# Performance work log

Measured on AMD Instinct MI355X. Metric: run time of the kernel, lower is better.

## Reference

```python
import jax, jax.numpy as jnp
import numpy as np

B, P, G, E = 2, 16, 128, 96
C110, C011, C001 = 4, 2, 1
N, CO = 128, 2

def _pw(x, W, b):
    """1x1 conv of any spatial rank == pointwise channel mixing."""
    y = jnp.einsum('oc,bc...->bo...', W, x)
    return y + b.reshape((1, -1) + (1,) * (y.ndim - 2))

def _hidden(s110, s011, s001, Ws, bs):
    # s110:[B,C,P,G,1]  s011:[B,C,1,G,E]  s001:[B,C,1,1,E]
    # sub-stream order: [110 full, 110 pool-P, 110 pool-G, 011 full, 011 pool-G, 011 pool-E, 001]
    t110 = s110[..., 0]         # [B,C,P,G]
    t011 = s011[:, :, 0]        # [B,C,G,E]
    t001 = s001[:, :, 0, 0]     # [B,C,E]
    s = (_pw(t110, Ws[0], bs[0])[..., None]
         + _pw(t110.max(axis=2), Ws[1], bs[1])[:, :, None, :, None]
         + _pw(t110.max(axis=3), Ws[2], bs[2])[:, :, :, None, None]
         + _pw(t011, Ws[3], bs[3])[:, :, None, :, :]
         + _pw(t011.max(axis=2), Ws[4], bs[4])[:, :, None, None, :]
         + _pw(t011.max(axis=3), Ws[5], bs[5])[:, :, None, :, None]
         + _pw(t001, Ws[6], bs[6])[:, :, None, None, :])
    s = jax.nn.leaky_relu(s)    # [B,N,P,G,E]
    return (jnp.max(s, axis=4, keepdims=True),
            jnp.max(s, axis=2, keepdims=True),
            jnp.max(s, axis=(2, 3), keepdims=True))

def _forward(x110, x011, x001, W0_110, b0_110, W0_011, b0_011, W0_001, b0_001, W1, b1, Wact, bact, Wcrit, bcrit):
    Ws0 = [W0_110[0], W0_110[1], W0_110[2], W0_011[0], W0_011[1], W0_011[2], W0_001]
    bs0 = [b0_110[0], b0_110[1], b0_110[2], b0_011[0], b0_011[1], b0_011[2], b0_001]
    s110, s011, s001 = _hidden(x110, x011, x001, Ws0, bs0)
    s110, s011, s001 = _hidden(s110, s011, s001, list(W1), list(b1))
    t110 = s110[..., 0]  # [B,N,P,G]
    # actor head: eliminate G,E via mean pooling (dim_elimination_max_pooling=False)
    a110 = _pw(t110.mean(axis=3), Wact[0], bact[0])              # [B,CO,P]
    a011 = _pw(s011.mean(axis=(3, 4)), Wact[1], bact[1])         # [B,CO,1]
    a001 = _pw(s001[:, :, :, 0].mean(axis=3), Wact[2], bact[2])  # [B,CO,1]
    actions = jax.nn.leaky_relu(a110 + a011 + a001)              # [B,CO,P]
    # critic head: eliminate G via mean pooling
    c110 = _pw(t110.mean(axis=3), Wcrit[0], bcrit[0])            # [B,CO,P]
    c011 = _pw(s011[:, :, 0].mean(axis=2), Wcrit[1], bcrit[1])   # [B,CO,E]
    c001 = _pw(s001[:, :, 0, 0], Wcrit[2], bcrit[2])             # [B,CO,E]
    v = jax.nn.leaky_relu(c110[:, :, :, None] + (c011 + c001)[:, :, None, :])  # [B,CO,P,E]
    v110 = v.max(axis=3).sum(axis=2)  # stream (1,1,0): max over E, sum over P
    v011 = v.max(axis=2).sum(axis=2)  # streams (0,1,1) and (0,0,1) coincide numerically
    values = (2.0 + v110 + 2.0 * v011).reshape(-1)  # python sum(l, 2) starts at 2
    return actions, values

def setup_inputs() -> dict:
    key = jax.random.key(0)
    ks = jax.random.split(key, 12)
    f32 = jnp.float32
    def w(k, shape, fan):
        return jax.random.normal(k, shape, f32) / np.float32(np.sqrt(fan))
    return {
        'x110': jax.random.normal(ks[0], (B, C110, P, G, 1), f32),
        'x011': jax.random.normal(ks[1], (B, C011, 1, G, E), f32),
        'x001': jax.random.normal(ks[2], (B, C001, 1, 1, E), f32),
        'W0_110': w(ks[3], (3, N, C110), C110), 'b0_110': jnp.zeros((3, N), f32),
        'W0_011': w(ks[4], (3, N, C011), C011), 'b0_011': jnp.zeros((3, N), f32),
        'W0_001': w(ks[5], (N, C001), C001),    'b0_001': jnp.zeros((N,), f32),
        'W1':     w(ks[6], (7, N, N), N),       'b1':     jnp.zeros((7, N), f32),
        'Wact':   w(ks[7], (3, CO, N), N),      'bact':   jnp.zeros((3, CO), f32),
        'Wcrit':  w(ks[8], (3, CO, N), N),      'bcrit':  jnp.zeros((3, CO), f32),
    }

def reference(x110, x011, x001, W0_110, b0_110, W0_011, b0_011, W0_001, b0_001, W1, b1, Wact, bact, Wcrit, bcrit):
    return _forward(x110, x011, x001, W0_110, b0_110, W0_011, b0_011, W0_001, b0_001, W1, b1, Wact, bact, Wcrit, bcrit)
```

## Files before the change

kernel.cpp:

```cpp
#include <hip/hip_runtime.h>
#include <math.h>

#define DEVI __device__ __forceinline__

constexpr int B = 2, P = 16, G = 128, E = 96, N = 128, CO = 2;

DEVI float lrelu(float x) { return x > 0.f ? x : 0.01f * x; }

constexpr int OFF_U1     = 0;
constexpr int OFF_V1     = OFF_U1 + 524288;
constexpr int OFF_MAXPU0 = OFF_V1 + 3145728;
constexpr int OFF_MAXEV0 = OFF_MAXPU0 + 32768;
constexpr int OFF_MP110  = OFF_MAXEV0 + 32768;
constexpr int OFF_MG110  = OFF_MP110 + 32768;
constexpr int OFF_S001A  = OFF_MG110 + 4096;
constexpr int OFF_RMP    = OFF_S001A + 24576;
constexpr int OFF_RMG    = OFF_RMP + 1024;
constexpr int OFF_RME    = OFF_RMG + 128;
constexpr int OFF_RMG011 = OFF_RME + 512;
constexpr int OFF_M110   = OFF_RMG011 + 384;
constexpr int OFF_M011E  = OFF_M110 + 4096;
constexpr int OFF_S001B  = OFF_M011E + 24576;
constexpr int OFF_WT     = OFF_S001B + 24576;

__global__ void __launch_bounds__(256) k_layer0(
    const float* __restrict__ x110, const float* __restrict__ x011,
    const float* __restrict__ x001,
    const float* __restrict__ W0_110, const float* __restrict__ b0_110,
    const float* __restrict__ W0_011, const float* __restrict__ b0_011,
    const float* __restrict__ W0_001, const float* __restrict__ b0_001,
    const float* __restrict__ W1,
    float* __restrict__ maxpU0g, float* __restrict__ maxeV0g,
    float* __restrict__ mp110, float* __restrict__ mg110,
    float* __restrict__ s001a,
    float* __restrict__ rmpG, float* __restrict__ rmgG,
    float* __restrict__ rmeG, float* __restrict__ rmg011G,
    float* __restrict__ wT) {
  __shared__ float xs[4 * 16 * 128];
  __shared__ float v0[128 * 97];
  __shared__ float u0[16 * 128];
  __shared__ float rmp[512], rmgS[64], rme[256], rmg011L[192];
  __shared__ float mpu[128], mev[128], part[256];
  const int bn = blockIdx.x, b = bn >> 7, n = bn & 127, tid = threadIdx.x;

  {
    const float4* xsrc = (const float4*)(x110 + (size_t)b * 8192);
    float4* xdst = (float4*)xs;
#pragma unroll
    for (int k = 0; k < 8; k++) xdst[tid + k * 256] = xsrc[tid + k * 256];
  }
  __syncthreads();
  for (int i = tid; i < 512; i += 256) {
    int c = i >> 7, g = i & 127;
    float m = -INFINITY;
    for (int p = 0; p < P; p++) m = fmaxf(m, xs[(c * 16 + p) * 128 + g]);
    rmp[i] = m;
  }
  if (tid < 64) {
    int c = tid >> 4, p = tid & 15;
    float m = -INFINITY;
    for (int g = 0; g < G; g++) m = fmaxf(m, xs[(c * 16 + p) * 128 + g]);
    rmgS[tid] = m;
  }
  {
    int c = tid >> 7, g = tid & 127;
    const float4* r = (const float4*)(x011 + ((size_t)(b * 2 + c) * 128 + g) * 96);
    float m = -INFINITY;
#pragma unroll
    for (int j = 0; j < 24; j++) {
      float4 v = r[j];
      m = fmaxf(m, fmaxf(fmaxf(v.x, v.y), fmaxf(v.z, v.w)));
    }
    rme[tid] = m;
  }
  if (tid < 192) {
    int c = tid / 96, e = tid % 96;
    const float* pp = x011 + ((size_t)(b * 2 + c) * 128) * 96 + e;
    float m = -INFINITY;
    for (int g = 0; g < G; g++) m = fmaxf(m, pp[g * 96]);
    rmg011L[tid] = m;
  }
  __syncthreads();
  float w0[4], w1[4], w2[4];
#pragma unroll
  for (int cc = 0; cc < 4; cc++) {
    w0[cc] = W0_110[n * 4 + cc];
    w1[cc] = W0_110[512 + n * 4 + cc];
    w2[cc] = W0_110[1024 + n * 4 + cc];
  }
  float we0 = W0_011[512 + n * 2], we1 = W0_011[512 + n * 2 + 1];
  float bu = b0_110[n] + b0_110[128 + n] + b0_110[256 + n] + b0_011[256 + n];
  float vw00 = W0_011[n * 2], vw01 = W0_011[n * 2 + 1];
  float vw10 = W0_011[256 + n * 2], vw11 = W0_011[256 + n * 2 + 1];
  float w001 = W0_001[n];
  float bv = b0_011[n] + b0_011[128 + n] + b0_001[n];

#pragma unroll
  for (int k = 0; k < 8; k++) {
    int i = tid + k * 256, p = i >> 7, g = i & 127;
    float acc = bu + we0 * rme[g] + we1 * rme[128 + g];
#pragma unroll
    for (int cc = 0; cc < 4; cc++)
      acc += w0[cc] * xs[(cc * 16 + p) * 128 + g] + w1[cc] * rmp[cc * 128 + g]
           + w2[cc] * rmgS[cc * 16 + p];
    u0[i] = acc;
  }
  {
    const float* xa = x011 + (size_t)(b * 2) * 12288;
    const float* xb = xa + 12288;
    const float* xc = x001 + b * 96;
    for (int k = 0; k < 48; k++) {
      int i = tid + k * 256;
      int g = i / 96, e = i - g * 96;
      float val = bv + vw00 * xa[i] + vw01 * xb[i]
                + vw10 * rmg011L[e] + vw11 * rmg011L[96 + e] + w001 * xc[e];
      v0[g * 97 + e] = val;
    }
  }
  __syncthreads();
  if (tid < 128) {
    float m = -INFINITY;
    for (int p = 0; p < P; p++) m = fmaxf(m, u0[p * 128 + tid]);
    mpu[tid] = m;
    maxpU0g[bn * 128 + tid] = m;
  }
  {
    int g = tid & 127, h = tid >> 7;
    const float* r = &v0[g * 97 + h * 48];
    float m = -INFINITY;
    for (int j = 0; j < 48; j++) m = fmaxf(m, r[j]);
    part[tid] = m;
  }
  __syncthreads();
  if (tid < 128) {
    float m = fmaxf(part[tid], part[128 + tid]);
    mev[tid] = m;
    maxeV0g[bn * 128 + tid] = m;
    mp110[bn * 128 + tid] = lrelu(mpu[tid] + m);
  }
  __syncthreads();
  {
    int p = tid >> 4, ch = tid & 15;
    float m = -INFINITY;
    for (int g = ch * 8; g < ch * 8 + 8; g++)
      m = fmaxf(m, u0[p * 128 + g] + mev[g]);
    part[tid] = m;
  }
  if (tid < 96) {
    float m = -INFINITY;
    for (int g = 0; g < G; g++) m = fmaxf(m, mpu[g] + v0[g * 97 + tid]);
    s001a[bn * 96 + tid] = lrelu(m);
  }
  __syncthreads();
  if (tid < 16) {
    float m = -INFINITY;
    for (int ch = 0; ch < 16; ch++) m = fmaxf(m, part[tid * 16 + ch]);
    mg110[bn * 16 + tid] = lrelu(m);
  }
  if (n == 0) {
    for (int i = tid; i < 512; i += 256) rmpG[b * 512 + i] = rmp[i];
    if (tid < 64) rmgG[b * 64 + tid] = rmgS[tid];
    rmeG[b * 256 + tid] = rme[tid];
    if (tid < 192) rmg011G[b * 192 + tid] = rmg011L[tid];
  }
  {
    const int gt = bn * 256 + tid;
#pragma unroll
    for (int it = 0; it < 2; it++) {
      int idx = gt + it * 65536;
      if (idx < 81920) {
        int m = idx >> 14, r = idx & 16383;
        int c = r >> 7, nn = r & 127;
        float v;
        if (m == 0)      v = W1[nn * 128 + c];
        else if (m == 1) v = W1[16384 + nn * 128 + c] + W1[5 * 16384 + nn * 128 + c];
        else if (m == 2) v = W1[2 * 16384 + nn * 128 + c];
        else if (m == 3) v = W1[3 * 16384 + nn * 128 + c];
        else             v = W1[4 * 16384 + nn * 128 + c] + W1[6 * 16384 + nn * 128 + c];
        wT[idx] = v;
      }
    }
  }
}

__global__ void __launch_bounds__(512) k_layer1c(
    const float* __restrict__ x110, const float* __restrict__ x011,
    const float* __restrict__ x001,
    const float* __restrict__ W0_110, const float* __restrict__ b0_110,
    const float* __restrict__ W0_011, const float* __restrict__ b0_011,
    const float* __restrict__ W0_001, const float* __restrict__ b0_001,
    const float* __restrict__ maxpU0g, const float* __restrict__ maxeV0g,
    const float* __restrict__ rmpG, const float* __restrict__ rmgG,
    const float* __restrict__ rmeG, const float* __restrict__ rmg011G,
    const float* __restrict__ wT,
    float* __restrict__ U1, float* __restrict__ V1) {
  __shared__ float s110c[128 * 16];
  __shared__ float s011c[128 * 96];
  __shared__ float W0L110[1536], W0L011[768], W0L001[128];
  __shared__ float busum[128], bvsum[128], mpu[128], mev[128];
  __shared__ float x011row[192], rmg011s[192], x001s[96];
  __shared__ float x110col[64], rmg110p[64], rmp4[4], rme2[2];
  const int blk = blockIdx.x;
  const int b = blk >> 7, g = blk & 127;
  const int tid = threadIdx.x;

  for (int i = tid; i < 1536; i += 512) W0L110[i] = W0_110[i];
  for (int i = tid; i < 768; i += 512) W0L011[i] = W0_011[i];
  if (tid < 128) {
    W0L001[tid] = W0_001[tid];
    busum[tid] = b0_110[tid] + b0_110[128 + tid] + b0_110[256 + tid]
               + b0_011[256 + tid];
    bvsum[tid] = b0_011[tid] + b0_011[128 + tid] + b0_001[tid];
    mpu[tid] = maxpU0g[(b * 128 + tid) * 128 + g];
    mev[tid] = maxeV0g[(b * 128 + tid) * 128 + g];
  } else if (tid >= 256 && tid < 448) {
    int i = tid - 256;
    int c = i / 96, e = i % 96;
    x011row[i] = x011[((size_t)(b * 2 + c) * 128 + g) * 96 + e];
    rmg011s[i] = rmg011G[b * 192 + i];
  } else if (tid >= 448 && tid < 512) {
    int i = tid - 448;
    int c = i >> 4, p = i & 15;
    x110col[i] = x110[((size_t)(b * 4 + c) * 16 + p) * 128 + g];
    rmg110p[i] = rmgG[b * 64 + i];
  } else if (tid >= 128 && tid < 224) {
    x001s[tid - 128] = x001[b * 96 + tid - 128];
  } else if (tid >= 224 && tid < 228) {
    rmp4[tid - 224] = rmpG[(b * 4 + tid - 224) * 128 + g];
  } else if (tid >= 228 && tid < 230) {
    rme2[tid - 228] = rmeG[(b * 2 + tid - 228) * 128 + g];
  }
  __syncthreads();

#pragma unroll
  for (int k = 0; k < 4; k++) {
    int i = tid + k * 512, c = i >> 4, p = i & 15;
    float acc = busum[c] + W0L011[512 + c * 2] * rme2[0]
              + W0L011[512 + c * 2 + 1] * rme2[1];
#pragma unroll
    for (int cc = 0; cc < 4; cc++)
      acc += W0L110[c * 4 + cc] * x110col[cc * 16 + p]
           + W0L110[512 + c * 4 + cc] * rmp4[cc]
           + W0L110[1024 + c * 4 + cc] * rmg110p[cc * 16 + p];
    s110c[i] = lrelu(acc + mev[c]);
  }
  for (int k = 0; k < 24; k++) {
    int i = tid + k * 512;
    int c = i / 96, e = i - c * 96;
    float v = bvsum[c]
            + W0L011[c * 2] * x011row[e] + W0L011[c * 2 + 1] * x011row[96 + e]
            + W0L011[256 + c * 2] * rmg011s[e]
            + W0L011[256 + c * 2 + 1] * rmg011s[96 + e]
            + W0L001[c] * x001s[e];
    s011c[i] = lrelu(v + mpu[c]);
  }
  __syncthreads();

  const float* w0T = wT;
  const float* w3T = wT + 3 * 16384;

  {
    int n = tid & 127, ph = tid >> 7;
    float a[4] = {0.f, 0.f, 0.f, 0.f};
    for (int c = 0; c < 128; c++) {
      float w0v = w0T[c * 128 + n];
      float4 s = *(const float4*)&s110c[c * 16 + ph * 4];
      a[0] += w0v * s.x; a[1] += w0v * s.y; a[2] += w0v * s.z; a[3] += w0v * s.w;
    }
    float* dst = U1 + ((size_t)((b * 128 + g) * 16 + ph * 4)) * 128 + n;
#pragma unroll
    for (int j = 0; j < 4; j++) dst[j * 128] = a[j];
  }
  {
    int n0 = (tid >> 3) * 2, e0 = (tid & 7) * 12;
    float4 aA[3], aB[3];
#pragma unroll
    for (int k = 0; k < 3; k++) {
      aA[k] = make_float4(0.f, 0.f, 0.f, 0.f);
      aB[k] = make_float4(0.f, 0.f, 0.f, 0.f);
    }
    for (int c = 0; c < 128; c++) {
      float2 wv = *(const float2*)&w3T[c * 128 + n0];
      float4 s0 = *(const float4*)&s011c[c * 96 + e0];
      float4 s1 = *(const float4*)&s011c[c * 96 + e0 + 4];
      float4 s2 = *(const float4*)&s011c[c * 96 + e0 + 8];
      aA[0].x += wv.x * s0.x; aA[0].y += wv.x * s0.y;
      aA[0].z += wv.x * s0.z; aA[0].w += wv.x * s0.w;
      aA[1].x += wv.x * s1.x; aA[1].y += wv.x * s1.y;
      aA[1].z += wv.x * s1.z; aA[1].w += wv.x * s1.w;
      aA[2].x += wv.x * s2.x; aA[2].y += wv.x * s2.y;
      aA[2].z += wv.x * s2.z; aA[2].w += wv.x * s2.w;
      aB[0].x += wv.y * s0.x; aB[0].y += wv.y * s0.y;
      aB[0].z += wv.y * s0.z; aB[0].w += wv.y * s0.w;
      aB[1].x += wv.y * s1.x; aB[1].y += wv.y * s1.y;
      aB[1].z += wv.y * s1.z; aB[1].w += wv.y * s1.w;
      aB[2].x += wv.y * s2.x; aB[2].y += wv.y * s2.y;
      aB[2].z += wv.y * s2.z; aB[2].w += wv.y * s2.w;
    }
    float* dA = V1 + ((size_t)((b * 128 + g) * 128 + n0)) * 96 + e0;
    float* dB = dA + 96;
#pragma unroll
    for (int k = 0; k < 3; k++) {
      *(float4*)(dA + k * 4) = aA[k];
      *(float4*)(dB + k * 4) = aB[k];
    }
  }
}

__global__ void __launch_bounds__(256) k_post1b(
    const float* __restrict__ U1, const float* __restrict__ V1,
    const float* __restrict__ s001a, const float* __restrict__ mp110,
    const float* __restrict__ mg110,
    const float* __restrict__ wT, const float* __restrict__ b1,
    float* __restrict__ m110, float* __restrict__ m011e,
    float* __restrict__ s001b) {
  __shared__ float vrow[128 * 97];
  __shared__ float uU[16 * 128];
  __shared__ float part[256];
  __shared__ float smaxeV[128], smaxpU[128];
  __shared__ float bf[128], eg[96], cp[16];
  const int bn = blockIdx.x, b = bn >> 7, n = bn & 127;
  const int tid = threadIdx.x;
  const float* w15T = wT + 16384;
  const float* w2T  = wT + 2 * 16384;
  const float* w46T = wT + 4 * 16384;

  if (tid < 128) {
    float acc = 0.f;
    for (int c = 0; c < 128; c++)
      acc += w15T[c * 128 + n] * mp110[(b * 128 + c) * 128 + tid];
    bf[tid] = acc;
  } else if (tid < 224) {
    int e = tid - 128;
    float acc = 0.f;
    for (int c = 0; c < 128; c++)
      acc += w46T[c * 128 + n] * s001a[b * 12288 + c * 96 + e];
    eg[e] = acc;
  } else if (tid < 240) {
    int p = tid - 224;
    float acc = 0.f;
    for (int c = 0; c < 128; c++)
      acc += w2T[c * 128 + n] * mg110[(b * 128 + c) * 16 + p];
    cp[p] = acc;
  }
  __syncthreads();
  const float bb = b1[n] + b1[128 + n] + b1[256 + n] + b1[640 + n];
  const float bv = b1[384 + n] + b1[512 + n] + b1[768 + n];

  for (int i = tid; i < 2048; i += 256) {
    int p = i >> 7, g = i & 127;
    uU[i] = U1[((size_t)((b * 128 + g) * 16 + p)) * 128 + n] + bb + cp[p] + bf[g];
  }
#pragma unroll
  for (int k = 0; k < 12; k++) {
    int i4 = tid + k * 256;
    int g = i4 / 24, e4 = i4 - g * 24;
    float4 v = *(const float4*)(V1 + ((size_t)((b * 128 + g) * 128 + n)) * 96 + e4 * 4);
    float* d = &vrow[g * 97 + e4 * 4];
    d[0] = v.x + bv + eg[e4 * 4];
    d[1] = v.y + bv + eg[e4 * 4 + 1];
    d[2] = v.z + bv + eg[e4 * 4 + 2];
    d[3] = v.w + bv + eg[e4 * 4 + 3];
  }
  __syncthreads();
  {
    int g = tid & 127, h = tid >> 7;
    const float* r = &vrow[g * 97 + h * 48];
    float m = -INFINITY;
    for (int j = 0; j < 48; j++) m = fmaxf(m, r[j]);
    part[tid] = m;
  }
  __syncthreads();
  if (tid < 128) {
    smaxeV[tid] = fmaxf(part[tid], part[tid + 128]);
    float mp = -INFINITY;
    for (int p = 0; p < P; p++) mp = fmaxf(mp, uU[p * 128 + tid]);
    smaxpU[tid] = mp;
  }
  __syncthreads();
  if (tid >= 128 && tid < 144) {
    int p = tid - 128;
    float s = 0.f;
    for (int g = 0; g < G; g++)
      s += lrelu(uU[p * 128 + g] + smaxeV[g]);
    m110[bn * 16 + p] = s * (1.f / G);
  }
  if (tid < 96) {
    float s = 0.f, mm = -INFINITY;
    for (int g = 0; g < G; g++) {
      float pre = smaxpU[g] + vrow[g * 97 + tid];
      s += lrelu(pre);
      mm = fmaxf(mm, pre);
    }
    m011e[bn * 96 + tid] = s * (1.f / G);
    s001b[bn * 96 + tid] = lrelu(mm);
  }
}

__global__ void __launch_bounds__(128) k_final(const float* __restrict__ m110,
                                               const float* __restrict__ m011e,
                                               const float* __restrict__ s001,
                                               const float* __restrict__ Wact,
                                               const float* __restrict__ bact,
                                               const float* __restrict__ Wcrit,
                                               const float* __restrict__ bcrit,
                                               float* __restrict__ out) {
  __shared__ float sm011[N], sm001[N], scp[P], sce[E], srow[P], scol[E];
  const int bo = blockIdx.x;
  const int o = bo & 1, b = bo >> 1;
  const int t = threadIdx.x;
  {
    float s1 = 0.f, s2 = 0.f;
    const float* p1 = m011e + (b * N + t) * E;
    const float* p2 = s001 + (b * N + t) * E;
    for (int e = 0; e < E; e++) { s1 += p1[e]; s2 += p2[e]; }
    sm011[t] = s1 * (1.f / E);
    sm001[t] = s2 * (1.f / E);
  }
  __syncthreads();
  if (t < P) {
    const float* wa0 = Wact + o * N;
    const float* wa1 = Wact + (1 * CO + o) * N;
    const float* wa2 = Wact + (2 * CO + o) * N;
    const float* wc0 = Wcrit + o * N;
    float a = 0.f, c = 0.f, aa = 0.f;
    for (int n = 0; n < N; n++) {
      float m = m110[(b * N + n) * P + t];
      a += wa0[n] * m;
      c += wc0[n] * m;
      aa += wa1[n] * sm011[n] + wa2[n] * sm001[n];
    }
    float act = a + aa + bact[o] + bact[CO + o] + bact[2 * CO + o];
    out[(b * CO + o) * P + t] = lrelu(act);
    scp[t] = c + bcrit[o];
  } else if (t < P + E) {
    int e = t - P;
    const float* wc1 = Wcrit + (1 * CO + o) * N;
    const float* wc2 = Wcrit + (2 * CO + o) * N;
    float c = 0.f;
    for (int n = 0; n < N; n++)
      c += wc1[n] * m011e[(b * N + n) * E + e] + wc2[n] * s001[(b * N + n) * E + e];
    sce[e] = c + bcrit[CO + o] + bcrit[2 * CO + o];
  }
  __syncthreads();
  if (t < P) {
    float m = -INFINITY;
    for (int e = 0; e < E; e++) m = fmaxf(m, lrelu(scp[t] + sce[e]));
    srow[t] = m;
  } else if (t < P + E) {
    int e = t - P;
    float m = -INFINITY;
    for (int p = 0; p < P; p++) m = fmaxf(m, lrelu(scp[p] + sce[e]));
    scol[e] = m;
  }
  __syncthreads();
  if (t == 0) {
    float v110 = 0.f, v011 = 0.f;
    for (int p = 0; p < P; p++) v110 += srow[p];
    for (int e = 0; e < E; e++) v011 += scol[e];
    out[B * CO * P + b * CO + o] = 2.f + v110 + 2.f * v011;
  }
}

extern "C" void kernel_launch(void* const* d_in, const int* in_sizes, int n_in,
                              void* d_out, int out_size, void* d_ws, size_t ws_size,
                              hipStream_t stream) {
  const float* x110   = (const float*)d_in[0];
  const float* x011   = (const float*)d_in[1];
  const float* x001   = (const float*)d_in[2];
  const float* W0_110 = (const float*)d_in[3];
  const float* b0_110 = (const float*)d_in[4];
  const float* W0_011 = (const float*)d_in[5];
  const float* b0_011 = (const float*)d_in[6];
  const float* W0_001 = (const float*)d_in[7];
  const float* b0_001 = (const float*)d_in[8];
  const float* W1     = (const float*)d_in[9];
  const float* b1     = (const float*)d_in[10];
  const float* Wact   = (const float*)d_in[11];
  const float* bact   = (const float*)d_in[12];
  const float* Wcrit  = (const float*)d_in[13];
  const float* bcrit  = (const float*)d_in[14];
  float* out = (float*)d_out;
  float* w = (float*)d_ws;

  float* U1     = w + OFF_U1;
  float* V1     = w + OFF_V1;
  float* maxpU0 = w + OFF_MAXPU0;
  float* maxeV0 = w + OFF_MAXEV0;
  float* mp110  = w + OFF_MP110;
  float* mg110  = w + OFF_MG110;
  float* s001a  = w + OFF_S001A;
  float* rmpG   = w + OFF_RMP;
  float* rmgG   = w + OFF_RMG;
  float* rmeG   = w + OFF_RME;
  float* rmg011 = w + OFF_RMG011;
  float* m110   = w + OFF_M110;
  float* m011e  = w + OFF_M011E;
  float* s001b  = w + OFF_S001B;
  float* wT     = w + OFF_WT;

  k_layer0<<<256, 256, 0, stream>>>(x110, x011, x001, W0_110, b0_110, W0_011,
                                    b0_011, W0_001, b0_001, W1,
                                    maxpU0, maxeV0, mp110, mg110, s001a,
                                    rmpG, rmgG, rmeG, rmg011, wT);
  k_layer1c<<<256, 512, 0, stream>>>(x110, x011, x001, W0_110, b0_110, W0_011,
                                     b0_011, W0_001, b0_001,
                                     maxpU0, maxeV0, rmpG, rmgG, rmeG, rmg011,
                                     wT, U1, V1);
  k_post1b<<<256, 256, 0, stream>>>(U1, V1, s001a, mp110, mg110, wT, b1,
                                    m110, m011e, s001b);
  k_final<<<4, 128, 0, stream>>>(m110, m011e, s001b, Wact, bact, Wcrit, bcrit, out);
}
```

Measured before the change: 108.5 us.

## Restructure post-layer kernel to tile 8 channels per block and stage k_final loads in LDS

The per-(b,n) post-processing kernel, which launched 256 blocks each reading a strided 128x96 V1 slice, is replaced by 32 blocks that each handle 8 consecutive channels. They stream G in chunks of 8 through shared memory, so V1 reads become contiguous across n, and they keep running sum and max accumulators in registers. The final kernel now stages m110, m011e and s001 in LDS with coalesced loads instead of doing strided per-thread global reads. The trade is far fewer blocks on a large GPU (32 vs 256), less parallelism and more syncs per block.

```diff
diff --git a/kernel.cpp b/kernel.cpp
--- a/kernel.cpp
+++ b/kernel.cpp
@@ -307,93 +307,128 @@
   }
 }
 
-__global__ void __launch_bounds__(256) k_post1b(
+__global__ void __launch_bounds__(256) k_post2(
     const float* __restrict__ U1, const float* __restrict__ V1,
     const float* __restrict__ s001a, const float* __restrict__ mp110,
     const float* __restrict__ mg110,
     const float* __restrict__ wT, const float* __restrict__ b1,
     float* __restrict__ m110, float* __restrict__ m011e,
     float* __restrict__ s001b) {
-  __shared__ float vrow[128 * 97];
-  __shared__ float uU[16 * 128];
-  __shared__ float part[256];
-  __shared__ float smaxeV[128], smaxpU[128];
-  __shared__ float bf[128], eg[96], cp[16];
-  const int bn = blockIdx.x, b = bn >> 7, n = bn & 127;
+  constexpr int GS = 8;
+  __shared__ float Vt[GS][8][100];
+  __shared__ float Ut[GS][16][9];
+  __shared__ float bfL[8][128];
+  __shared__ float egL[8][96];
+  __shared__ float cpL[8][16];
+  __shared__ float partE[GS][8][4];
+  __shared__ float mxeV[GS][8], mxpU[GS][8];
+  __shared__ float bbL[8], bvL[8];
+  const int blk = blockIdx.x, b = blk >> 4, nc = blk & 15, n0 = nc * 8;
   const int tid = threadIdx.x;
   const float* w15T = wT + 16384;
   const float* w2T  = wT + 2 * 16384;
   const float* w46T = wT + 4 * 16384;
 
-  if (tid < 128) {
+  if (tid < 8) {
+    int n = n0 + tid;
+    bbL[tid] = b1[n] + b1[128 + n] + b1[256 + n] + b1[640 + n];
+    bvL[tid] = b1[384 + n] + b1[512 + n] + b1[768 + n];
+  }
+  {
+    int g = tid & 127, h = tid >> 7;
+    float a0 = 0, a1 = 0, a2 = 0, a3 = 0;
+    for (int c = 0; c < 128; c++) {
+      float m = mp110[(b * 128 + c) * 128 + g];
+      const float* wr = &w15T[c * 128 + n0 + h * 4];
+      a0 += wr[0] * m; a1 += wr[1] * m; a2 += wr[2] * m; a3 += wr[3] * m;
+    }
+    bfL[h * 4 + 0][g] = a0; bfL[h * 4 + 1][g] = a1;
+    bfL[h * 4 + 2][g] = a2; bfL[h * 4 + 3][g] = a3;
+  }
+#pragma unroll
+  for (int k = 0; k < 3; k++) {
+    int s = tid + k * 256;
+    int nn = s / 96, e = s % 96;
     float acc = 0.f;
     for (int c = 0; c < 128; c++)
-      acc += w15T[c * 128 + n] * mp110[(b * 128 + c) * 128 + tid];
-    bf[tid] = acc;
-  } else if (tid < 224) {
-    int e = tid - 128;
+      acc += w46T[c * 128 + n0 + nn] * s001a[b * 12288 + c * 96 + e];
+    egL[nn][e] = acc;
+  }
+  if (tid < 128) {
+    int nn = tid >> 4, p = tid & 15;
     float acc = 0.f;
     for (int c = 0; c < 128; c++)
-      acc += w46T[c * 128 + n] * s001a[b * 12288 + c * 96 + e];
-    eg[e] = acc;
-  } else if (tid < 240) {
-    int p = tid - 224;
-    float acc = 0.f;
-    for (int c = 0; c < 128; c++)
-      acc += w2T[c * 128 + n] * mg110[(b * 128 + c) * 16 + p];
-    cp[p] = acc;
-  }
-  __syncthreads();
-  const float bb = b1[n] + b1[128 + n] + b1[256 + n] + b1[640 + n];
-  const float bv = b1[384 + n] + b1[512 + n] + b1[768 + n];
-
-  for (int i = tid; i < 2048; i += 256) {
-    int p = i >> 7, g = i & 127;
-    uU[i] = U1[((size_t)((b * 128 + g) * 16 + p)) * 128 + n] + bb + cp[p] + bf[g];
-  }
-#pragma unroll
-  for (int k = 0; k < 12; k++) {
-    int i4 = tid + k * 256;
-    int g = i4 / 24, e4 = i4 - g * 24;
-    float4 v = *(const float4*)(V1 + ((size_t)((b * 128 + g) * 128 + n)) * 96 + e4 * 4);
-    float* d = &vrow[g * 97 + e4 * 4];
-    d[0] = v.x + bv + eg[e4 * 4];
-    d[1] = v.y + bv + eg[e4 * 4 + 1];
-    d[2] = v.z + bv + eg[e4 * 4 + 2];
-    d[3] = v.w + bv + eg[e4 * 4 + 3];
-  }
-  __syncthreads();
-  {
-    int g = tid & 127, h = tid >> 7;
-    const float* r = &vrow[g * 97 + h * 48];
-    float m = -INFINITY;
-    for (int j = 0; j < 48; j++) m = fmaxf(m, r[j]);
-    part[tid] = m;
-  }
-  __syncthreads();
+      acc += w2T[c * 128 + n0 + nn] * mg110[(b * 128 + c) * 16 + p];
+    cpL[nn][p] = acc;
+  }
+
+  float accM110 = 0.f;
+  float accSum[3] = {0.f, 0.f, 0.f};
+  float accMax[3] = {-INFINITY, -INFINITY, -INFINITY};
+  const size_t Ubase = (size_t)b * 128 * 16 * 128;
+  const size_t Vbase = (size_t)b * 128 * 128 * 96;
+
+  for (int go = 0; go < 128; go += GS) {
+    __syncthreads();
+#pragma unroll
+    for (int k = 0; k < 24; k++) {
+      int i = tid + k * 256;
+      int gs = i / 768, r = i % 768, nn = r / 96, e = r % 96;
+      float v = V1[Vbase + ((size_t)(go + gs) * 128 + n0 + nn) * 96 + e];
+      Vt[gs][nn][e] = v + bvL[nn] + egL[nn][e];
+    }
+#pragma unroll
+    for (int k = 0; k < 4; k++) {
+      int i = tid + k * 256;
+      int gs = i >> 7, r = i & 127, p = r >> 3, nn = r & 7;
+      float u = U1[Ubase + ((size_t)(go + gs) * 16 + p) * 128 + n0 + nn];
+      Ut[gs][p][nn] = u + bbL[nn] + cpL[nn][p] + bfL[nn][go + gs];
+    }
+    __syncthreads();
+    {
+      int gs = tid >> 5, nn = (tid >> 2) & 7, ec = tid & 3;
+      float m = -INFINITY;
+      for (int e = ec * 24; e < ec * 24 + 24; e++) m = fmaxf(m, Vt[gs][nn][e]);
+      partE[gs][nn][ec] = m;
+    }
+    __syncthreads();
+    if (tid < 64) {
+      int gs = tid >> 3, nn = tid & 7;
+      mxeV[gs][nn] = fmaxf(fmaxf(partE[gs][nn][0], partE[gs][nn][1]),
+                           fmaxf(partE[gs][nn][2], partE[gs][nn][3]));
+      float m = -INFINITY;
+      for (int p = 0; p < 16; p++) m = fmaxf(m, Ut[gs][p][nn]);
+      mxpU[gs][nn] = m;
+    }
+    __syncthreads();
+    if (tid < 128) {
+      int nn = tid >> 4, p = tid & 15;
+#pragma unroll
+      for (int gs = 0; gs < GS; gs++)
+        accM110 += lrelu(Ut[gs][p][nn] + mxeV[gs][nn]);
+    }
+#pragma unroll
+    for (int k = 0; k < 3; k++) {
+      int s = tid + k * 256;
+      int nn = s / 96, e = s % 96;
+#pragma unroll
+      for (int gs = 0; gs < GS; gs++) {
+        float pre = mxpU[gs][nn] + Vt[gs][nn][e];
+        accSum[k] += lrelu(pre);
+        accMax[k] = fmaxf(accMax[k], pre);
+      }
+    }
+  }
   if (tid < 128) {
-    smaxeV[tid] = fmaxf(part[tid], part[tid + 128]);
-    float mp = -INFINITY;
-    for (int p = 0; p < P; p++) mp = fmaxf(mp, uU[p * 128 + tid]);
-    smaxpU[tid] = mp;
-  }
-  __syncthreads();
-  if (tid >= 128 && tid < 144) {
-    int p = tid - 128;
-    float s = 0.f;
-    for (int g = 0; g < G; g++)
-      s += lrelu(uU[p * 128 + g] + smaxeV[g]);
-    m110[bn * 16 + p] = s * (1.f / G);
-  }
-  if (tid < 96) {
-    float s = 0.f, mm = -INFINITY;
-    for (int g = 0; g < G; g++) {
-      float pre = smaxpU[g] + vrow[g * 97 + tid];
-      s += lrelu(pre);
-      mm = fmaxf(mm, pre);
-    }
-    m011e[bn * 96 + tid] = s * (1.f / G);
-    s001b[bn * 96 + tid] = lrelu(mm);
+    int nn = tid >> 4, p = tid & 15;
+    m110[(b * 128 + n0 + nn) * 16 + p] = accM110 * (1.f / G);
+  }
+#pragma unroll
+  for (int k = 0; k < 3; k++) {
+    int s = tid + k * 256;
+    int nn = s / 96, e = s % 96;
+    m011e[(b * 128 + n0 + nn) * 96 + e] = accSum[k] * (1.f / G);
+    s001b[(b * 128 + n0 + nn) * 96 + e] = lrelu(accMax[k]);
   }
 }
 
@@ -405,17 +440,50 @@
                                                const float* __restrict__ Wcrit,
                                                const float* __restrict__ bcrit,
                                                float* __restrict__ out) {
-  __shared__ float sm011[N], sm001[N], scp[P], sce[E], srow[P], scol[E];
+  __shared__ float buf[128][97];
+  __shared__ float m110s[128][17];
+  __shared__ float sm011[N], sm001[N], sce1[E], sce[E], scp[P], srow[P], scol[E];
   const int bo = blockIdx.x;
   const int o = bo & 1, b = bo >> 1;
   const int t = threadIdx.x;
-  {
-    float s1 = 0.f, s2 = 0.f;
-    const float* p1 = m011e + (b * N + t) * E;
-    const float* p2 = s001 + (b * N + t) * E;
-    for (int e = 0; e < E; e++) { s1 += p1[e]; s2 += p2[e]; }
-    sm011[t] = s1 * (1.f / E);
-    sm001[t] = s2 * (1.f / E);
+
+#pragma unroll
+  for (int k = 0; k < 16; k++) {
+    int i = t + k * 128;
+    m110s[i >> 4][i & 15] = m110[b * 2048 + i];
+  }
+  for (int k = 0; k < 96; k++) {
+    int i = t + k * 128;
+    buf[i / 96][i % 96] = m011e[b * 12288 + i];
+  }
+  __syncthreads();
+  {
+    float s = 0.f;
+    for (int e = 0; e < E; e++) s += buf[t][e];
+    sm011[t] = s * (1.f / E);
+  }
+  if (t < 96) {
+    const float* wc1 = Wcrit + (1 * CO + o) * N;
+    float c = 0.f;
+    for (int n = 0; n < N; n++) c += wc1[n] * buf[n][t];
+    sce1[t] = c;
+  }
+  __syncthreads();
+  for (int k = 0; k < 96; k++) {
+    int i = t + k * 128;
+    buf[i / 96][i % 96] = s001[b * 12288 + i];
+  }
+  __syncthreads();
+  {
+    float s = 0.f;
+    for (int e = 0; e < E; e++) s += buf[t][e];
+    sm001[t] = s * (1.f / E);
+  }
+  if (t < 96) {
+    const float* wc2 = Wcrit + (2 * CO + o) * N;
+    float c = 0.f;
+    for (int n = 0; n < N; n++) c += wc2[n] * buf[n][t];
+    sce[t] = sce1[t] + c + bcrit[CO + o] + bcrit[2 * CO + o];
   }
   __syncthreads();
   if (t < P) {
@@ -425,7 +493,7 @@
     const float* wc0 = Wcrit + o * N;
     float a = 0.f, c = 0.f, aa = 0.f;
     for (int n = 0; n < N; n++) {
-      float m = m110[(b * N + n) * P + t];
+      float m = m110s[n][t];
       a += wa0[n] * m;
       c += wc0[n] * m;
       aa += wa1[n] * sm011[n] + wa2[n] * sm001[n];
@@ -433,14 +501,6 @@
     float act = a + aa + bact[o] + bact[CO + o] + bact[2 * CO + o];
     out[(b * CO + o) * P + t] = lrelu(act);
     scp[t] = c + bcrit[o];
-  } else if (t < P + E) {
-    int e = t - P;
-    const float* wc1 = Wcrit + (1 * CO + o) * N;
-    const float* wc2 = Wcrit + (2 * CO + o) * N;
-    float c = 0.f;
-    for (int n = 0; n < N; n++)
-      c += wc1[n] * m011e[(b * N + n) * E + e] + wc2[n] * s001[(b * N + n) * E + e];
-    sce[e] = c + bcrit[CO + o] + bcrit[2 * CO + o];
   }
   __syncthreads();
   if (t < P) {
@@ -507,7 +567,7 @@
                                      b0_011, W0_001, b0_001,
                                      maxpU0, maxeV0, rmpG, rmgG, rmeG, rmg011,
                                      wT, U1, V1);
-  k_post1b<<<256, 256, 0, stream>>>(U1, V1, s001a, mp110, mg110, wT, b1,
-                                    m110, m011e, s001b);
+  k_post2<<<32, 256, 0, stream>>>(U1, V1, s001a, mp110, mg110, wT, b1,
+                                  m110, m011e, s001b);
   k_final<<<4, 128, 0, stream>>>(m110, m011e, s001b, Wact, bact, Wcrit, bcrit, out);
 }
```

New measurement: 145.5 us. 34.1% more time.
